# Performance work log

Measured on AMD Instinct MI355X. Metric: run time of the kernel, lower is better.

Reference implementation:

```python
import jax, jax.numpy as jnp
import numpy as np

B, E, H, S, V, K = 128, 512, 512, 2048, 83, 3
PAD = 82


def _pos_emb(n, e):
    pos = jnp.arange(n, dtype=jnp.float32)[:, None]                      # [n,1]
    k = jnp.exp(-jnp.log(10000.0) * jnp.arange(0, e, 2, dtype=jnp.float32) / e)  # [e/2]
    arg = pos * k                                                        # [n,e/2]
    pe = jnp.stack([jnp.sin(arg), jnp.cos(arg)], axis=-1).reshape(n, e)  # interleave sin/cos
    return pe.T                                                          # [e,n]


def setup_inputs() -> dict:
    key = jax.random.key(0)
    ks = jax.random.split(key, 8)
    return {
        "encoder_output": jax.random.normal(ks[0], (B, H, S), dtype=jnp.float32),
        "encoder_total": jax.random.normal(ks[1], (B, H, S), dtype=jnp.float32),
        "decoder_input": jax.random.randint(ks[2], (B,), 0, V),
        "count": 0,
        "emb": jax.random.normal(ks[3], (V, E), dtype=jnp.float32) * 0.02,
        "conv_w": jax.random.normal(ks[4], (2 * H, E, K), dtype=jnp.float32) * 0.02,
        "conv_b": jnp.zeros((2 * H,), dtype=jnp.float32),
        "lin2_w": jax.random.normal(ks[5], (V, H), dtype=jnp.float32) * 0.02,
        "lin2_b": jnp.zeros((V,), dtype=jnp.float32),
    }


def reference(encoder_output, encoder_total, decoder_input, count, emb, conv_w, conv_b, lin2_w, lin2_b):
    # count==0 first-step path; dropout is identity (inference).
    pe3 = _pos_emb(K, E)                                    # [E,K]

    def layer(dec_in):
        # dec_in: [B,E,K]
        xp = dec_in + pe3[None]                             # positional embedding add
        y = jnp.einsum('bek,oek->bo', xp, conv_w) + conv_b  # valid conv1d, out length 1 -> [B,2H]
        a, b = jnp.split(y, 2, axis=1)
        glu = a * jax.nn.sigmoid(b)                         # [B,H]
        d = glu + xp[:, :, -1]                              # residual with last (pe-added) column
        scores = jnp.einsum('bh,bhs->bs', d, encoder_output)
        attn = jax.nn.softmax(scores, axis=-1)              # [B,S]
        c = jnp.einsum('bs,bhs->bh', attn, encoder_total)   # [B,H]
        h = glu + c
        logits = h @ lin2_w.T + lin2_b                      # [B,V]
        return h, jax.nn.log_softmax(logits, axis=-1)

    x = emb[decoder_input][:, :, None]                      # [B,E,1]
    pad_col = jnp.broadcast_to(emb[PAD][None, :, None], (B, E, 1))
    dec1 = jnp.concatenate([pad_col, pad_col, x], axis=2)   # [B,E,3]

    h1, _ = layer(dec1)                                     # n_l = 0
    dec2 = jnp.concatenate([dec1[:, :, :2], h1[:, :, None]], axis=2)
    h2, _ = layer(dec2)                                     # n_l = 1
    dec3 = jnp.concatenate([dec1[:, :, :2], h2[:, :, None]], axis=2)
    h3, ls3 = layer(dec3)                                   # n_l = 2

    return (jax.nn.softmax(h3, axis=1)[:, :, None],         # [B,H,1]
            ls3[:, None, :])                                # [B,1,V]
```

## Files before the change

kernel.cpp:

```cpp
#include <hip/hip_runtime.h>
#include <math.h>

#define B_   128
#define E_   512
#define H_   512
#define S_   2048
#define V_   83
#define PAD_ 82

typedef float v4f __attribute__((ext_vector_type(4)));

__device__ __forceinline__ v4f ldnt4(const float* p) {
    return __builtin_nontemporal_load((const v4f*)p);
}


__global__ void k_misc(const float* __restrict__ emb, float* __restrict__ pe2,
                       float* __restrict__ x01i) {
    int e = threadIdx.x;
    float freq = expf(-9.210340371976184f * (float)(e & ~1) * (1.0f / 512.0f));
    float p0 = (e & 1) ? 1.0f : 0.0f;
    float p1 = (e & 1) ? cosf(freq) : sinf(freq);
    float p2 = (e & 1) ? cosf(2.0f * freq) : sinf(2.0f * freq);
    pe2[e] = p2;
    float ep = emb[PAD_ * 512 + e];
    x01i[e * 3 + 0] = ep + p0;
    x01i[e * 3 + 1] = ep + p1;
    x01i[e * 3 + 2] = 0.0f;
}

__global__ void k_base3(const float* __restrict__ cw, const float* __restrict__ x01i,
                        float* __restrict__ base) {
    int t = threadIdx.x, w = t >> 6, lane = t & 63;
    __shared__ float xs[1536];
    for (int j = t; j < 1536; j += 256) xs[j] = x01i[j];
    __syncthreads();
    int o = blockIdx.x * 4 + w;
    const float* rp = cw + (size_t)o * 1536 + lane * 4;
    float acc = 0.f;
    #pragma unroll
    for (int j = 0; j < 6; ++j) {
        float4 v = *(const float4*)(rp + j * 256);
        const float* xp = &xs[lane * 4 + j * 256];
        acc += v.x * xp[0] + v.y * xp[1] + v.z * xp[2] + v.w * xp[3];
    }
    #pragma unroll
    for (int off = 32; off > 0; off >>= 1) acc += __shfl_down(acc, off, 64);
    if (lane == 0) base[o] = acc;
}

__global__ void k_prep(const float* __restrict__ cw, float* __restrict__ W2t) {
    __shared__ float tile[64][129];
    int ob = blockIdx.x * 64, eb = blockIdx.y * 128;
    int t = threadIdx.x;
    for (int idx = t; idx < 8192; idx += 256) {
        int r = idx >> 7, e = idx & 127;
        tile[r][e] = cw[(size_t)(ob + r) * 1536 + (eb + e) * 3 + 2];
    }
    __syncthreads();
    for (int idx = t; idx < 8192; idx += 256) {
        int e = idx >> 6, o = idx & 63;
        W2t[(size_t)(eb + e) * 1024 + ob + o] = tile[o][e];
    }
}


__global__ void k_yx(int first, const int* __restrict__ tok, const float* __restrict__ emb,
                     const float* __restrict__ h, const float* __restrict__ pe2,
                     const float* __restrict__ W2t, const float* __restrict__ base,
                     const float* __restrict__ cb, float* __restrict__ xcol,
                     float* __restrict__ y) {
    int oc = blockIdx.x, bq = blockIdx.y, t = threadIdx.x;
    __shared__ float xs[4][512];
    for (int j = t; j < 2048; j += 256) {
        int bb = j >> 9, e = j & 511;
        int b = bq * 4 + bb;
        float v = first ? emb[tok[b] * 512 + e] : h[b * 512 + e];
        xs[bb][e] = v + pe2[e];
    }
    __syncthreads();
    if (oc == 0)
        for (int j = t; j < 2048; j += 256) xcol[bq * 2048 + j] = xs[j >> 9][j & 511];
    int o = oc * 256 + t;
    float init = base[o] + cb[o];
    float a0 = init, a1 = init, a2 = init, a3 = init;
    for (int e = 0; e < 512; ++e) {
        float w = W2t[e * 1024 + o];
        a0 += xs[0][e] * w; a1 += xs[1][e] * w;
        a2 += xs[2][e] * w; a3 += xs[3][e] * w;
    }
    int b0 = bq * 4;
    y[(size_t)(b0 + 0) * 1024 + o] = a0;
    y[(size_t)(b0 + 1) * 1024 + o] = a1;
    y[(size_t)(b0 + 2) * 1024 + o] = a2;
    y[(size_t)(b0 + 3) * 1024 + o] = a3;
}

__global__ void k_scores2(const float* __restrict__ y, const float* __restrict__ xcol,
                          const float* __restrict__ enc, float* __restrict__ part) {
    int hc = blockIdx.x, b = blockIdx.y, t = threadIdx.x;
    int w = t >> 6, lane = t & 63;
    __shared__ float dl[64];
    __shared__ float red[4 * 2048];
    if (t < 64) {
        int hg = hc * 64 + t;
        float ya = y[b * 1024 + hg];
        float yb_ = y[b * 1024 + 512 + hg];
        float g = ya / (1.0f + expf(-yb_));
        dl[t] = g + xcol[b * 512 + hg];
    }
    __syncthreads();
    v4f a[8];
    #pragma unroll
    for (int j = 0; j < 8; ++j) a[j] = (v4f)(0.f);
    const float* bp = enc + ((size_t)b * 512 + hc * 64 + w * 16) * 2048 + lane * 4;
    for (int r = 0; r < 16; ++r) {
        float dh = dl[w * 16 + r];
        const float* rp = bp + (size_t)r * 2048;
        #pragma unroll
        for (int j = 0; j < 8; ++j) {
            v4f v = ldnt4(rp + j * 256);
            a[j] += dh * v;
        }
    }
    #pragma unroll
    for (int j = 0; j < 8; ++j)
        *(v4f*)&red[w * 2048 + j * 256 + lane * 4] = a[j];
    __syncthreads();
    #pragma unroll
    for (int k = 0; k < 2; ++k) {
        int s = t * 4 + k * 1024;
        v4f s0 = *(const v4f*)&red[0 * 2048 + s];
        v4f s1 = *(const v4f*)&red[1 * 2048 + s];
        v4f s2 = *(const v4f*)&red[2 * 2048 + s];
        v4f s3 = *(const v4f*)&red[3 * 2048 + s];
        *(v4f*)&part[(size_t)hc * 262144 + b * 2048 + s] = (s0 + s1) + (s2 + s3);
    }
}

__global__ void k_softmax2(const float* __restrict__ part, float* __restrict__ attn) {
    int b = blockIdx.x, t = threadIdx.x;
    float v[8];
    float m = -1e30f;
    for (int i = 0; i < 8; ++i) {
        int s = i * 256 + t;
        float acc = 0.f;
        #pragma unroll
        for (int hc = 0; hc < 8; ++hc) acc += part[(size_t)hc * 262144 + b * 2048 + s];
        v[i] = acc; m = fmaxf(m, acc);
    }
    __shared__ float r[256];
    r[t] = m; __syncthreads();
    for (int s = 128; s > 0; s >>= 1) { if (t < s) r[t] = fmaxf(r[t], r[t + s]); __syncthreads(); }
    float M = r[0]; __syncthreads();
    float sum = 0.f;
    for (int i = 0; i < 8; ++i) { v[i] = expf(v[i] - M); sum += v[i]; }
    r[t] = sum; __syncthreads();
    for (int s = 128; s > 0; s >>= 1) { if (t < s) r[t] += r[t + s]; __syncthreads(); }
    float inv = 1.0f / r[0];
    for (int i = 0; i < 8; ++i) attn[b * 2048 + i * 256 + t] = v[i] * inv;
}

__global__ void k_c2(const float* __restrict__ attn, const float* __restrict__ enc,
                     const float* __restrict__ y, float* __restrict__ hbuf) {
    int t = threadIdx.x;
    int b  = blockIdx.x >> 7;
    int h0 = (blockIdx.x & 127) << 2;
    __shared__ float al[2048];
    for (int j = t; j < 2048; j += 256) al[j] = attn[b * 2048 + j];
    __syncthreads();
    int w = t >> 6, lane = t & 63;
    int hh = h0 + w;
    const float* vp = enc + ((size_t)b * 512 + hh) * 2048;
    float acc = 0.f;
    #pragma unroll
    for (int it = 0; it < 8; ++it) {
        int s = it * 256 + lane * 4;
        v4f v = ldnt4(vp + s);
        float4 p = *(const float4*)&al[s];
        acc += p.x * v[0] + p.y * v[1] + p.z * v[2] + p.w * v[3];
    }
    #pragma unroll
    for (int off = 32; off > 0; off >>= 1) acc += __shfl_down(acc, off, 64);
    if (lane == 0) {
        float ya = y[b * 1024 + hh];
        float yb_ = y[b * 1024 + 512 + hh];
        float g = ya / (1.0f + expf(-yb_));
        hbuf[b * 512 + hh] = g + acc;
    }
}


__global__ void k_epi(const float* __restrict__ h, const float* __restrict__ l2w,
                      const float* __restrict__ l2b, float* __restrict__ out) {
    int b = blockIdx.x, t = threadIdx.x;
    __shared__ float hl[512];
    hl[t] = h[b * 512 + t]; hl[t + 256] = h[b * 512 + 256 + t];
    __syncthreads();
    float acc = 0.f;
    if (t < V_) {
        acc = l2b[t];
        for (int e = 0; e < 512; ++e) acc += hl[e] * l2w[t * 512 + e];
    }
    __shared__ float r[256];
    r[t] = (t < V_) ? acc : -1e30f; __syncthreads();
    for (int s = 128; s > 0; s >>= 1) { if (t < s) r[t] = fmaxf(r[t], r[t + s]); __syncthreads(); }
    float M = r[0]; __syncthreads();
    r[t] = (t < V_) ? expf(acc - M) : 0.f; __syncthreads();
    for (int s = 128; s > 0; s >>= 1) { if (t < s) r[t] += r[t + s]; __syncthreads(); }
    float L = M + logf(r[0]);
    if (t < V_) out[65536 + b * V_ + t] = acc - L;
    __syncthreads();
    float v0 = hl[t], v1 = hl[t + 256];
    r[t] = fmaxf(v0, v1); __syncthreads();
    for (int s = 128; s > 0; s >>= 1) { if (t < s) r[t] = fmaxf(r[t], r[t + s]); __syncthreads(); }
    float M2 = r[0]; __syncthreads();
    float e0 = expf(v0 - M2), e1 = expf(v1 - M2);
    r[t] = e0 + e1; __syncthreads();
    for (int s = 128; s > 0; s >>= 1) { if (t < s) r[t] += r[t + s]; __syncthreads(); }
    float inv = 1.0f / r[0];
    out[b * 512 + t] = e0 * inv;
    out[b * 512 + 256 + t] = e1 * inv;
}


extern "C" void kernel_launch(void* const* d_in, const int* in_sizes, int n_in,
                              void* d_out, int out_size, void* d_ws, size_t ws_size,
                              hipStream_t stream) {
    const float* enc_out = (const float*)d_in[0];
    const float* enc_tot = (const float*)d_in[1];
    const int*   tok     = (const int*)d_in[2];
    const float* emb     = (const float*)d_in[4];
    const float* conv_w  = (const float*)d_in[5];
    const float* conv_b  = (const float*)d_in[6];
    const float* l2w     = (const float*)d_in[7];
    const float* l2b     = (const float*)d_in[8];
    float* out = (float*)d_out;
    float* ws = (float*)d_ws;

    float* W2t  = ws;
    float* base = W2t + 524288;
    float* pe2  = base + 1024;
    float* x01i = pe2 + 512;
    float* xcol = x01i + 1536;
    float* yb   = xcol + 65536;
    float* attn = yb + 131072;
    float* part = attn + 262144;
    float* hbuf = part + 2097152;

    k_misc<<<1, 512, 0, stream>>>(emb, pe2, x01i);
    k_base3<<<256, 256, 0, stream>>>(conv_w, x01i, base);
    k_prep<<<dim3(16, 4), 256, 0, stream>>>(conv_w, W2t);

    for (int L = 0; L < 3; ++L) {
        k_yx<<<dim3(4, 32), 256, 0, stream>>>(L == 0 ? 1 : 0, tok, emb, hbuf, pe2,
                                              W2t, base, conv_b, xcol, yb);
        k_scores2<<<dim3(8, 128), 256, 0, stream>>>(yb, xcol, enc_out, part);
        k_softmax2<<<128, 256, 0, stream>>>(part, attn);
        k_c2<<<16384, 256, 0, stream>>>(attn, enc_tot, yb, hbuf);
    }

    k_epi<<<128, 256, 0, stream>>>(hbuf, l2w, l2b, out);
}
```

Before: 630.2 us.

## Fuse conv GLU projection into scores kernel and split hidden dim finer

Removes the separate conv-projection kernel k_yx and computes each block's 32 GLU outputs inside the scores kernel, using wave-level dot products over an untransposed weight copy. The scores pass now splits H into 16 chunks per batch row with no shared-memory cross-wave reduction, so each wave writes its own slice of the S partials. Softmax sums 16 partials with vector loads, and the c kernel reads the precomputed GLU. This saves one launch and the y round trip per layer. In exchange the conv weights are re-read by every batch block (128x redundancy, mostly from cache) and the partial buffer doubles in size.

```diff
diff --git a/kernel.cpp b/kernel.cpp
--- a/kernel.cpp
+++ b/kernel.cpp
@@ -30,7 +30,7 @@
 }
 
 __global__ void k_base3(const float* __restrict__ cw, const float* __restrict__ x01i,
-                        float* __restrict__ base) {
+                        const float* __restrict__ cb, float* __restrict__ bc) {
     int t = threadIdx.x, w = t >> 6, lane = t & 63;
     __shared__ float xs[1536];
     for (int j = t; j < 1536; j += 256) xs[j] = x01i[j];
@@ -46,123 +46,100 @@
     }
     #pragma unroll
     for (int off = 32; off > 0; off >>= 1) acc += __shfl_down(acc, off, 64);
-    if (lane == 0) base[o] = acc;
-}
-
-__global__ void k_prep(const float* __restrict__ cw, float* __restrict__ W2t) {
-    __shared__ float tile[64][129];
-    int ob = blockIdx.x * 64, eb = blockIdx.y * 128;
-    int t = threadIdx.x;
-    for (int idx = t; idx < 8192; idx += 256) {
-        int r = idx >> 7, e = idx & 127;
-        tile[r][e] = cw[(size_t)(ob + r) * 1536 + (eb + e) * 3 + 2];
-    }
-    __syncthreads();
-    for (int idx = t; idx < 8192; idx += 256) {
-        int e = idx >> 6, o = idx & 63;
-        W2t[(size_t)(eb + e) * 1024 + ob + o] = tile[o][e];
-    }
-}
-
-
-__global__ void k_yx(int first, const int* __restrict__ tok, const float* __restrict__ emb,
-                     const float* __restrict__ h, const float* __restrict__ pe2,
-                     const float* __restrict__ W2t, const float* __restrict__ base,
-                     const float* __restrict__ cb, float* __restrict__ xcol,
-                     float* __restrict__ y) {
-    int oc = blockIdx.x, bq = blockIdx.y, t = threadIdx.x;
-    __shared__ float xs[4][512];
-    for (int j = t; j < 2048; j += 256) {
-        int bb = j >> 9, e = j & 511;
-        int b = bq * 4 + bb;
-        float v = first ? emb[tok[b] * 512 + e] : h[b * 512 + e];
-        xs[bb][e] = v + pe2[e];
-    }
-    __syncthreads();
-    if (oc == 0)
-        for (int j = t; j < 2048; j += 256) xcol[bq * 2048 + j] = xs[j >> 9][j & 511];
-    int o = oc * 256 + t;
-    float init = base[o] + cb[o];
-    float a0 = init, a1 = init, a2 = init, a3 = init;
-    for (int e = 0; e < 512; ++e) {
-        float w = W2t[e * 1024 + o];
-        a0 += xs[0][e] * w; a1 += xs[1][e] * w;
-        a2 += xs[2][e] * w; a3 += xs[3][e] * w;
-    }
-    int b0 = bq * 4;
-    y[(size_t)(b0 + 0) * 1024 + o] = a0;
-    y[(size_t)(b0 + 1) * 1024 + o] = a1;
-    y[(size_t)(b0 + 2) * 1024 + o] = a2;
-    y[(size_t)(b0 + 3) * 1024 + o] = a3;
-}
-
-__global__ void k_scores2(const float* __restrict__ y, const float* __restrict__ xcol,
-                          const float* __restrict__ enc, float* __restrict__ part) {
+    if (lane == 0) bc[o] = acc + cb[o];
+}
+
+__global__ void k_prepc(const float* __restrict__ cw, float* __restrict__ Wc) {
+    int idx = blockIdx.x * 256 + threadIdx.x;
+    int o = idx >> 9, e = idx & 511;
+    Wc[idx] = cw[o * 1536 + e * 3 + 2];
+}
+
+
+__global__ void __launch_bounds__(256) k_syx(
+        int first, const int* __restrict__ tok, const float* __restrict__ emb,
+        const float* __restrict__ hbuf, const float* __restrict__ pe2,
+        const float* __restrict__ Wc, const float* __restrict__ bc,
+        const float* __restrict__ eo, float* __restrict__ glu,
+        float* __restrict__ part) {
     int hc = blockIdx.x, b = blockIdx.y, t = threadIdx.x;
     int w = t >> 6, lane = t & 63;
-    __shared__ float dl[64];
-    __shared__ float red[4 * 2048];
-    if (t < 64) {
-        int hg = hc * 64 + t;
-        float ya = y[b * 1024 + hg];
-        float yb_ = y[b * 1024 + 512 + hg];
-        float g = ya / (1.0f + expf(-yb_));
-        dl[t] = g + xcol[b * 512 + hg];
-    }
-    __syncthreads();
-    v4f a[8];
-    #pragma unroll
-    for (int j = 0; j < 8; ++j) a[j] = (v4f)(0.f);
-    const float* bp = enc + ((size_t)b * 512 + hc * 64 + w * 16) * 2048 + lane * 4;
-    for (int r = 0; r < 16; ++r) {
-        float dh = dl[w * 16 + r];
+    __shared__ float xs[512];
+    __shared__ float dl[32];
+    for (int e = t; e < 512; e += 256) {
+        float v = first ? emb[tok[b] * 512 + e] : hbuf[b * 512 + e];
+        xs[e] = v + pe2[e];
+    }
+    __syncthreads();
+    for (int r = 0; r < 8; ++r) {
+        int hg = hc * 32 + w * 8 + r;
+        const float* wa = Wc + (size_t)hg * 512;
+        const float* wb = Wc + (size_t)(512 + hg) * 512;
+        float pa = 0.f, pb = 0.f;
+        #pragma unroll
+        for (int k = 0; k < 8; ++k) {
+            int e = lane + k * 64;
+            float x = xs[e];
+            pa += wa[e] * x;
+            pb += wb[e] * x;
+        }
+        #pragma unroll
+        for (int off = 32; off > 0; off >>= 1) {
+            pa += __shfl_xor(pa, off, 64);
+            pb += __shfl_xor(pb, off, 64);
+        }
+        if (lane == 0) {
+            float ya = pa + bc[hg];
+            float yb = pb + bc[512 + hg];
+            float g = ya / (1.0f + expf(-yb));
+            glu[b * 512 + hg] = g;
+            dl[w * 8 + r] = g + xs[hg];
+        }
+    }
+    __syncthreads();
+    v4f a0 = (v4f)(0.f), a1 = (v4f)(0.f);
+    const float* bp = eo + ((size_t)b * 512 + hc * 32) * 2048 + w * 512 + lane * 4;
+    for (int r = 0; r < 32; ++r) {
+        float dh = dl[r];
         const float* rp = bp + (size_t)r * 2048;
-        #pragma unroll
-        for (int j = 0; j < 8; ++j) {
-            v4f v = ldnt4(rp + j * 256);
-            a[j] += dh * v;
-        }
-    }
-    #pragma unroll
-    for (int j = 0; j < 8; ++j)
-        *(v4f*)&red[w * 2048 + j * 256 + lane * 4] = a[j];
-    __syncthreads();
-    #pragma unroll
-    for (int k = 0; k < 2; ++k) {
-        int s = t * 4 + k * 1024;
-        v4f s0 = *(const v4f*)&red[0 * 2048 + s];
-        v4f s1 = *(const v4f*)&red[1 * 2048 + s];
-        v4f s2 = *(const v4f*)&red[2 * 2048 + s];
-        v4f s3 = *(const v4f*)&red[3 * 2048 + s];
-        *(v4f*)&part[(size_t)hc * 262144 + b * 2048 + s] = (s0 + s1) + (s2 + s3);
-    }
+        a0 += dh * ldnt4(rp);
+        a1 += dh * ldnt4(rp + 256);
+    }
+    float* pp = part + (size_t)hc * 262144 + b * 2048 + w * 512 + lane * 4;
+    *(v4f*)pp = a0;
+    *(v4f*)(pp + 256) = a1;
 }
 
 __global__ void k_softmax2(const float* __restrict__ part, float* __restrict__ attn) {
     int b = blockIdx.x, t = threadIdx.x;
-    float v[8];
-    float m = -1e30f;
-    for (int i = 0; i < 8; ++i) {
-        int s = i * 256 + t;
-        float acc = 0.f;
-        #pragma unroll
-        for (int hc = 0; hc < 8; ++hc) acc += part[(size_t)hc * 262144 + b * 2048 + s];
-        v[i] = acc; m = fmaxf(m, acc);
-    }
+    v4f v0 = (v4f)(0.f), v1 = (v4f)(0.f);
+    #pragma unroll
+    for (int hc = 0; hc < 16; ++hc) {
+        const float* pp = part + (size_t)hc * 262144 + b * 2048 + t * 4;
+        v0 += *(const v4f*)pp;
+        v1 += *(const v4f*)(pp + 1024);
+    }
+    float m = fmaxf(fmaxf(fmaxf(v0[0], v0[1]), fmaxf(v0[2], v0[3])),
+                    fmaxf(fmaxf(v1[0], v1[1]), fmaxf(v1[2], v1[3])));
     __shared__ float r[256];
     r[t] = m; __syncthreads();
     for (int s = 128; s > 0; s >>= 1) { if (t < s) r[t] = fmaxf(r[t], r[t + s]); __syncthreads(); }
     float M = r[0]; __syncthreads();
+    v4f e0, e1;
     float sum = 0.f;
-    for (int i = 0; i < 8; ++i) { v[i] = expf(v[i] - M); sum += v[i]; }
+    #pragma unroll
+    for (int i = 0; i < 4; ++i) { e0[i] = expf(v0[i] - M); sum += e0[i]; }
+    #pragma unroll
+    for (int i = 0; i < 4; ++i) { e1[i] = expf(v1[i] - M); sum += e1[i]; }
     r[t] = sum; __syncthreads();
     for (int s = 128; s > 0; s >>= 1) { if (t < s) r[t] += r[t + s]; __syncthreads(); }
     float inv = 1.0f / r[0];
-    for (int i = 0; i < 8; ++i) attn[b * 2048 + i * 256 + t] = v[i] * inv;
+    *(v4f*)&attn[b * 2048 + t * 4] = e0 * inv;
+    *(v4f*)&attn[b * 2048 + 1024 + t * 4] = e1 * inv;
 }
 
 __global__ void k_c2(const float* __restrict__ attn, const float* __restrict__ enc,
-                     const float* __restrict__ y, float* __restrict__ hbuf) {
+                     const float* __restrict__ glu, float* __restrict__ hbuf) {
     int t = threadIdx.x;
     int b  = blockIdx.x >> 7;
     int h0 = (blockIdx.x & 127) << 2;
@@ -182,12 +159,7 @@
     }
     #pragma unroll
     for (int off = 32; off > 0; off >>= 1) acc += __shfl_down(acc, off, 64);
-    if (lane == 0) {
-        float ya = y[b * 1024 + hh];
-        float yb_ = y[b * 1024 + 512 + hh];
-        float g = ya / (1.0f + expf(-yb_));
-        hbuf[b * 512 + hh] = g + acc;
-    }
+    if (lane == 0) hbuf[b * 512 + hh] = glu[b * 512 + hh] + acc;
 }
 
 
@@ -238,26 +210,24 @@
     float* out = (float*)d_out;
     float* ws = (float*)d_ws;
 
-    float* W2t  = ws;
-    float* base = W2t + 524288;
-    float* pe2  = base + 1024;
+    float* Wc   = ws;
+    float* bc   = Wc + 524288;
+    float* pe2  = bc + 1024;
     float* x01i = pe2 + 512;
-    float* xcol = x01i + 1536;
-    float* yb   = xcol + 65536;
-    float* attn = yb + 131072;
-    float* part = attn + 262144;
-    float* hbuf = part + 2097152;
+    float* glu  = x01i + 1536;
+    float* part = glu + 65536;
+    float* attn = part + 4194304;
+    float* hbuf = attn + 262144;
 
     k_misc<<<1, 512, 0, stream>>>(emb, pe2, x01i);
-    k_base3<<<256, 256, 0, stream>>>(conv_w, x01i, base);
-    k_prep<<<dim3(16, 4), 256, 0, stream>>>(conv_w, W2t);
+    k_base3<<<256, 256, 0, stream>>>(conv_w, x01i, conv_b, bc);
+    k_prepc<<<2048, 256, 0, stream>>>(conv_w, Wc);
 
     for (int L = 0; L < 3; ++L) {
-        k_yx<<<dim3(4, 32), 256, 0, stream>>>(L == 0 ? 1 : 0, tok, emb, hbuf, pe2,
-                                              W2t, base, conv_b, xcol, yb);
-        k_scores2<<<dim3(8, 128), 256, 0, stream>>>(yb, xcol, enc_out, part);
+        k_syx<<<dim3(16, 128), 256, 0, stream>>>(L == 0 ? 1 : 0, tok, emb, hbuf, pe2,
+                                                 Wc, bc, enc_out, glu, part);
         k_softmax2<<<128, 256, 0, stream>>>(part, attn);
-        k_c2<<<16384, 256, 0, stream>>>(attn, enc_tot, yb, hbuf);
+        k_c2<<<16384, 256, 0, stream>>>(attn, enc_tot, glu, hbuf);
     }
 
     k_epi<<<128, 256, 0, stream>>>(hbuf, l2w, l2b, out);
```

Measured after the change: 583.0 us. -7.5%, faster.
